# Performance work log

Measured on AMD Instinct MI355X. Metric: run time of the kernel, lower is better.

Reference implementation:

```python
import jax, jax.numpy as jnp
import numpy as np

SIGMA_MAX = 0.3
GAMMA = 1.0
COV_SHRINK = 0.1
COV_DELTA = 1e-3
BN_EPS = 1e-5
PATCH = 3


def setup_inputs() -> dict:
    key = jax.random.key(0)
    ks = jax.random.split(key, 5)
    B, K, C, H, W = 2, 8, 64, 128, 128
    X = jax.random.normal(ks[0], (B, K, C, H, W), dtype=jnp.float32)
    w1 = jax.random.normal(ks[1], (C // 2, C), dtype=jnp.float32) * 0.1
    w2 = jax.random.normal(ks[2], (1, C // 2), dtype=jnp.float32) * 0.1
    return {
        "X": X,
        "w1": w1,
        "bn_scale": jnp.ones((C // 2,), jnp.float32),
        "bn_bias": jnp.zeros((C // 2,), jnp.float32),
        "bn_mean": jnp.zeros((C // 2,), jnp.float32),
        "bn_var": jnp.ones((C // 2,), jnp.float32),
        "w2": w2,
        "a0_raw": jax.random.normal(ks[3], (K,), dtype=jnp.float32) * 0.1,
        "sigma_raw": jax.random.normal(ks[4], (K,), dtype=jnp.float32) * 0.1,
    }


def _forward(X, w1, bn_scale, bn_bias, bn_mean, bn_var, w2, a0_raw, sigma_raw):
    B, K, C, H, W = X.shape
    # --- SensorMapGenerator: 1x1 conv -> BN (inference) -> ReLU -> 1x1 conv ---
    Xf = X.reshape(B * K, C, H, W)
    h = jnp.einsum('oc,bchw->bohw', w1, Xf)                       # [BK, C/2, H, W]
    inv_std = bn_scale / jnp.sqrt(bn_var + BN_EPS)
    h = h * inv_std[None, :, None, None] + (bn_bias - bn_mean * inv_std)[None, :, None, None]
    h = jax.nn.relu(h)
    S = jnp.einsum('oc,bchw->bohw', w2, h).reshape(B, K, H, W)    # scalar sensor maps

    # --- CovarianceEstimator: reflect pad, 3x3 patches, center, R = PP^T/N ---
    pad = PATCH // 2
    Sp = jnp.pad(S, ((0, 0), (0, 0), (pad, pad), (pad, pad)), mode='reflect')
    patches = jnp.stack(
        [Sp[:, :, i:i + H, j:j + W] for i in range(PATCH) for j in range(PATCH)],
        axis=-1)                                                  # [B, K, H, W, N]
    N = PATCH * PATCH
    patches = patches.transpose(0, 2, 3, 1, 4)                    # [B, H, W, K, N]
    pc = patches - patches.mean(axis=-1, keepdims=True)
    R = jnp.matmul(pc, pc.swapaxes(-1, -2)) / N                   # [B, H, W, K, K]

    # --- Guidance vector and uncertainty (stage mode) ---
    a0 = jax.nn.softmax(a0_raw)                                   # [K], sums to 1
    sigma = SIGMA_MAX * jax.nn.sigmoid(sigma_raw)                 # [K]

    # --- Robust diagonal-loaded Capon solve per pixel ---
    # R_reg = (1-shrink)*R + shrink*(tr R / K)*I + delta*I + gamma*diag(sigma^2)
    I = jnp.eye(K, dtype=R.dtype)
    tr = jnp.trace(R, axis1=-2, axis2=-1)                         # [B, H, W]
    load = COV_DELTA * I + GAMMA * jnp.diag(sigma * sigma)
    R_load = (1.0 - COV_SHRINK) * R + (COV_SHRINK * tr / K)[..., None, None] * I + load
    rhs = jnp.broadcast_to(a0[:, None], R_load.shape[:-2] + (K, 1))
    w_un = jnp.linalg.solve(R_load, rhs)[..., 0]                  # [B, H, W, K]
    denom = jnp.einsum('bhwk,k->bhw', w_un, a0)
    w = w_un / denom[..., None]                                   # a0^T w = 1

    # --- Weighted fusion over streams ---
    Y = jnp.einsum('bhwk,bkchw->bchw', w, X)                      # [B, C, H, W]
    return Y


def reference(X, w1, bn_scale, bn_bias, bn_mean, bn_var, w2, a0_raw, sigma_raw):
    return _forward(X, w1, bn_scale, bn_bias, bn_mean, bn_var, w2, a0_raw, sigma_raw)
```

## Files before the change

### kernel.cpp

```cpp
#include <hip/hip_runtime.h>
#include <hip/hip_bf16.h>
#include <math.h>

#define B_    2
#define K_    8
#define C_    64
#define CH_   32
#define H_    128
#define W_    128
#define HW_   16384
#define BN_EPS 1e-5f
#define SIGMA_MAX 0.3f
#define COV_SHRINK 0.1f
#define COV_DELTA 1e-3f

#define REP32(M) \
    M(0)  M(1)  M(2)  M(3)  M(4)  M(5)  M(6)  M(7)  \
    M(8)  M(9)  M(10) M(11) M(12) M(13) M(14) M(15) \
    M(16) M(17) M(18) M(19) M(20) M(21) M(22) M(23) \
    M(24) M(25) M(26) M(27) M(28) M(29) M(30) M(31)

__global__ void prep_kernel(const float* __restrict__ w1,
                            const float* __restrict__ bn_scale,
                            const float* __restrict__ bn_bias,
                            const float* __restrict__ bn_mean,
                            const float* __restrict__ bn_var,
                            const float* __restrict__ w2,
                            float* __restrict__ par) {
    int t = threadIdx.x;
    for (int i = t; i < CH_ * C_; i += blockDim.x) {
        int c = i >> 5;
        int o = i & 31;
        float inv = bn_scale[o] * rsqrtf(bn_var[o] + BN_EPS);
        par[c * CH_ + o] = w1[o * C_ + c] * inv;
    }
    if (t < CH_) {
        float inv = bn_scale[t] * rsqrtf(bn_var[t] + BN_EPS);
        par[2048 + t] = bn_bias[t] - bn_mean[t] * inv;
        par[2080 + t] = w2[t];
    }
}

__global__ void __launch_bounds__(256)
stage1_kernel(const float* __restrict__ X,
              const float* __restrict__ wf,
              const float* __restrict__ beff,
              const float* __restrict__ w2c,
              float* __restrict__ S) {
    int idx = blockIdx.x * blockDim.x + threadIdx.x;
    int hw = idx & (HW_ - 1);
    int bk = idx >> 14;
    const float* xp = X + (size_t)bk * (C_ * HW_) + hw;

#define DECL_ACC(o) float a##o = beff[o];
    REP32(DECL_ACC)
#undef DECL_ACC

#pragma unroll 2
    for (int c = 0; c < C_; ++c) {
        float xv = xp[(size_t)c * HW_];
        const float* wr = wf + c * CH_;
#define FMA_ONE(o) a##o = fmaf(wr[o], xv, a##o);
        REP32(FMA_ONE)
#undef FMA_ONE
    }

    float s = 0.f;
#define REDUCE_ONE(o) s = fmaf(w2c[o], fmaxf(a##o, 0.f), s);
    REP32(REDUCE_ONE)
#undef REDUCE_ONE
    S[idx] = s;
}

__global__ void capon_kernel(const float* __restrict__ S,
                             const float* __restrict__ a0_raw,
                             const float* __restrict__ sigma_raw,
                             float* __restrict__ wOut) {
    int idx = blockIdx.x * blockDim.x + threadIdx.x;
    int b  = idx >> 14;
    int hw = idx & (HW_ - 1);
    int h  = hw >> 7;
    int w  = hw & (W_ - 1);

    float a0[K_], sig2[K_];
    {
        float m = -1e30f;
#pragma unroll
        for (int i = 0; i < K_; ++i) m = fmaxf(m, a0_raw[i]);
        float sum = 0.f;
#pragma unroll
        for (int i = 0; i < K_; ++i) { a0[i] = __expf(a0_raw[i] - m); sum += a0[i]; }
        float invs = 1.f / sum;
#pragma unroll
        for (int i = 0; i < K_; ++i) a0[i] *= invs;
#pragma unroll
        for (int i = 0; i < K_; ++i) {
            float sg = SIGMA_MAX / (1.f + __expf(-sigma_raw[i]));
            sig2[i] = sg * sg;
        }
    }

    int hm = (h == 0)      ? 1       : h - 1;
    int hp = (h == H_ - 1) ? H_ - 2  : h + 1;
    int wm = (w == 0)      ? 1       : w - 1;
    int wp = (w == W_ - 1) ? W_ - 2  : w + 1;
    int rows[3] = {hm * W_, h * W_, hp * W_};
    int cols[3] = {wm, w, wp};

    float pc[K_][9];
#pragma unroll
    for (int k = 0; k < K_; ++k) {
        const float* sp = S + (((size_t)b * K_ + k) << 14);
        float p[9];
        float m = 0.f;
#pragma unroll
        for (int i = 0; i < 3; ++i)
#pragma unroll
            for (int j = 0; j < 3; ++j) {
                float v = sp[rows[i] + cols[j]];
                p[i * 3 + j] = v;
                m += v;
            }
        m *= (1.f / 9.f);
#pragma unroll
        for (int n = 0; n < 9; ++n) pc[k][n] = p[n] - m;
    }

    float A[K_][K_];
    float tr = 0.f;
#pragma unroll
    for (int i = 0; i < K_; ++i) {
        float s = 0.f;
#pragma unroll
        for (int n = 0; n < 9; ++n) s = fmaf(pc[i][n], pc[i][n], s);
        s *= (1.f / 9.f);
        tr += s;
        A[i][i] = s;
    }
#pragma unroll
    for (int i = 0; i < K_; ++i)
#pragma unroll
        for (int j = 0; j < i; ++j) {
            float s = 0.f;
#pragma unroll
            for (int n = 0; n < 9; ++n) s = fmaf(pc[i][n], pc[j][n], s);
            A[i][j] = (1.f - COV_SHRINK) * s * (1.f / 9.f);
        }
    float dl = COV_SHRINK * tr * (1.f / (float)K_) + COV_DELTA;
#pragma unroll
    for (int i = 0; i < K_; ++i)
        A[i][i] = (1.f - COV_SHRINK) * A[i][i] + dl + sig2[i];

#pragma unroll
    for (int j = 0; j < K_; ++j) {
        float d = A[j][j];
#pragma unroll
        for (int t = 0; t < j; ++t) d = fmaf(-A[j][t], A[j][t], d);
        d = sqrtf(d);
        A[j][j] = d;
        float inv = 1.f / d;
#pragma unroll
        for (int i = j + 1; i < K_; ++i) {
            float s = A[i][j];
#pragma unroll
            for (int t = 0; t < j; ++t) s = fmaf(-A[i][t], A[j][t], s);
            A[i][j] = s * inv;
        }
    }
    float z[K_];
#pragma unroll
    for (int i = 0; i < K_; ++i) {
        float s = a0[i];
#pragma unroll
        for (int t = 0; t < i; ++t) s = fmaf(-A[i][t], z[t], s);
        z[i] = s / A[i][i];
    }
    float x[K_];
#pragma unroll
    for (int i = K_ - 1; i >= 0; --i) {
        float s = z[i];
#pragma unroll
        for (int t = i + 1; t < K_; ++t) s = fmaf(-A[t][i], x[t], s);
        x[i] = s / A[i][i];
    }
    float denom = 0.f;
#pragma unroll
    for (int k = 0; k < K_; ++k) denom = fmaf(x[k], a0[k], denom);
    float invd = 1.f / denom;

    float4 o0 = make_float4(x[0] * invd, x[1] * invd, x[2] * invd, x[3] * invd);
    float4 o1 = make_float4(x[4] * invd, x[5] * invd, x[6] * invd, x[7] * invd);
    float4* dst = (float4*)(wOut + (size_t)idx * K_);
    dst[0] = o0;
    dst[1] = o1;
}

__global__ void __launch_bounds__(256)
fuse_kernel(const float* __restrict__ X,
            const float* __restrict__ wW,
            float* __restrict__ out) {
    int idx = blockIdx.x * blockDim.x + threadIdx.x;
    int hw = idx & (HW_ - 1);
    int bc = idx >> 14;
    int b = bc >> 6;
    int c = bc & (C_ - 1);
    size_t pix = ((size_t)b << 14) + hw;

    const float4* wv4 = (const float4*)(wW + pix * K_);
    float4 wa = wv4[0];
    float4 wb = wv4[1];

    const float* xp = X + (((size_t)b * K_) * C_ + c) * HW_ + hw;
    const size_t kstride = (size_t)C_ * HW_;

    float acc;
    acc = wa.x * xp[0];
    acc = fmaf(wa.y, xp[kstride * 1], acc);
    acc = fmaf(wa.z, xp[kstride * 2], acc);
    acc = fmaf(wa.w, xp[kstride * 3], acc);
    acc = fmaf(wb.x, xp[kstride * 4], acc);
    acc = fmaf(wb.y, xp[kstride * 5], acc);
    acc = fmaf(wb.z, xp[kstride * 6], acc);
    acc = fmaf(wb.w, xp[kstride * 7], acc);
    __builtin_nontemporal_store(acc, &out[idx]);
}

extern "C" void kernel_launch(void* const* d_in, const int* in_sizes, int n_in,
                              void* d_out, int out_size, void* d_ws, size_t ws_size,
                              hipStream_t stream) {
    const float* X         = (const float*)d_in[0];
    const float* w1        = (const float*)d_in[1];
    const float* bn_scale  = (const float*)d_in[2];
    const float* bn_bias   = (const float*)d_in[3];
    const float* bn_mean   = (const float*)d_in[4];
    const float* bn_var    = (const float*)d_in[5];
    const float* w2        = (const float*)d_in[6];
    const float* a0_raw    = (const float*)d_in[7];
    const float* sigma_raw = (const float*)d_in[8];
    float* out = (float*)d_out;
    float* ws  = (float*)d_ws;

    float* par = ws;
    float* S   = ws + 4096;
    float* wW  = ws + 4096 + (B_ * K_ * HW_);

    prep_kernel<<<1, 256, 0, stream>>>(w1, bn_scale, bn_bias, bn_mean, bn_var,
                                       w2, par);

    int n1 = B_ * K_ * HW_;
    stage1_kernel<<<n1 / 256, 256, 0, stream>>>(X, par, par + 2048, par + 2080, S);

    int n2 = B_ * HW_;
    capon_kernel<<<n2 / 64, 64, 0, stream>>>(S, a0_raw, sigma_raw, wW);

    int n3 = B_ * C_ * HW_;
    fuse_kernel<<<n3 / 256, 256, 0, stream>>>(X, wW, out);
}
```

Baseline: 141.0 us.

## Fuse Capon solve with stream fusion and process two pixels per stage1 thread

The Capon kernel now does the weighted fusion over streams itself. Each thread loops over all 64 channels, using its per-pixel weights kept in registers. This removes the separate fuse kernel launch and the round trip of the weight buffer through global memory. Stage1 is also changed so each thread handles two adjacent pixels with float2 loads, reusing each loaded weight for two FMAs. The risk is that the memory-bound fusion pass, which reads all of X, now runs on only 32K threads in 64-thread blocks, which may leave too few loads in flight to cover latency.

```diff
diff --git a/kernel.cpp b/kernel.cpp
--- a/kernel.cpp
+++ b/kernel.cpp
@@ -47,35 +47,38 @@
               const float* __restrict__ beff,
               const float* __restrict__ w2c,
               float* __restrict__ S) {
-    int idx = blockIdx.x * blockDim.x + threadIdx.x;
-    int hw = idx & (HW_ - 1);
-    int bk = idx >> 14;
-    const float* xp = X + (size_t)bk * (C_ * HW_) + hw;
-
-#define DECL_ACC(o) float a##o = beff[o];
+    int t = blockIdx.x * blockDim.x + threadIdx.x;
+    int hw2 = t & (HW_ / 2 - 1);
+    int bk  = t >> 13;
+    const float2* xp = (const float2*)(X + (size_t)bk * (C_ * HW_)) + hw2;
+
+#define DECL_ACC(o) float u##o = beff[o]; float v##o = u##o;
     REP32(DECL_ACC)
 #undef DECL_ACC
 
-#pragma unroll 2
+#pragma unroll 4
     for (int c = 0; c < C_; ++c) {
-        float xv = xp[(size_t)c * HW_];
+        float2 xv = xp[(size_t)c * (HW_ / 2)];
         const float* wr = wf + c * CH_;
-#define FMA_ONE(o) a##o = fmaf(wr[o], xv, a##o);
+#define FMA_ONE(o) u##o = fmaf(wr[o], xv.x, u##o); v##o = fmaf(wr[o], xv.y, v##o);
         REP32(FMA_ONE)
 #undef FMA_ONE
     }
 
-    float s = 0.f;
-#define REDUCE_ONE(o) s = fmaf(w2c[o], fmaxf(a##o, 0.f), s);
+    float s0 = 0.f, s1 = 0.f;
+#define REDUCE_ONE(o) \
+    s0 = fmaf(w2c[o], fmaxf(u##o, 0.f), s0); \
+    s1 = fmaf(w2c[o], fmaxf(v##o, 0.f), s1);
     REP32(REDUCE_ONE)
 #undef REDUCE_ONE
-    S[idx] = s;
-}
-
-__global__ void capon_kernel(const float* __restrict__ S,
-                             const float* __restrict__ a0_raw,
-                             const float* __restrict__ sigma_raw,
-                             float* __restrict__ wOut) {
+    ((float2*)S)[t] = make_float2(s0, s1);
+}
+
+__global__ void capon_fuse_kernel(const float* __restrict__ S,
+                                  const float* __restrict__ a0_raw,
+                                  const float* __restrict__ sigma_raw,
+                                  const float* __restrict__ X,
+                                  float* __restrict__ out) {
     int idx = blockIdx.x * blockDim.x + threadIdx.x;
     int b  = idx >> 14;
     int hw = idx & (HW_ - 1);
@@ -188,41 +191,27 @@
     for (int k = 0; k < K_; ++k) denom = fmaf(x[k], a0[k], denom);
     float invd = 1.f / denom;
 
-    float4 o0 = make_float4(x[0] * invd, x[1] * invd, x[2] * invd, x[3] * invd);
-    float4 o1 = make_float4(x[4] * invd, x[5] * invd, x[6] * invd, x[7] * invd);
-    float4* dst = (float4*)(wOut + (size_t)idx * K_);
-    dst[0] = o0;
-    dst[1] = o1;
-}
-
-__global__ void __launch_bounds__(256)
-fuse_kernel(const float* __restrict__ X,
-            const float* __restrict__ wW,
-            float* __restrict__ out) {
-    int idx = blockIdx.x * blockDim.x + threadIdx.x;
-    int hw = idx & (HW_ - 1);
-    int bc = idx >> 14;
-    int b = bc >> 6;
-    int c = bc & (C_ - 1);
-    size_t pix = ((size_t)b << 14) + hw;
-
-    const float4* wv4 = (const float4*)(wW + pix * K_);
-    float4 wa = wv4[0];
-    float4 wb = wv4[1];
-
-    const float* xp = X + (((size_t)b * K_) * C_ + c) * HW_ + hw;
-    const size_t kstride = (size_t)C_ * HW_;
-
-    float acc;
-    acc = wa.x * xp[0];
-    acc = fmaf(wa.y, xp[kstride * 1], acc);
-    acc = fmaf(wa.z, xp[kstride * 2], acc);
-    acc = fmaf(wa.w, xp[kstride * 3], acc);
-    acc = fmaf(wb.x, xp[kstride * 4], acc);
-    acc = fmaf(wb.y, xp[kstride * 5], acc);
-    acc = fmaf(wb.z, xp[kstride * 6], acc);
-    acc = fmaf(wb.w, xp[kstride * 7], acc);
-    __builtin_nontemporal_store(acc, &out[idx]);
+    float wk[K_];
+#pragma unroll
+    for (int k = 0; k < K_; ++k) wk[k] = x[k] * invd;
+
+    const float* xb = X + ((size_t)b * K_) * (C_ * HW_) + hw;
+    float* ob = out + ((size_t)b * C_) * HW_ + hw;
+    const size_t KS = (size_t)C_ * HW_;
+
+#pragma unroll 4
+    for (int c = 0; c < C_; ++c) {
+        const float* xc = xb + (size_t)c * HW_;
+        float acc = wk[0] * xc[0];
+        acc = fmaf(wk[1], xc[KS * 1], acc);
+        acc = fmaf(wk[2], xc[KS * 2], acc);
+        acc = fmaf(wk[3], xc[KS * 3], acc);
+        acc = fmaf(wk[4], xc[KS * 4], acc);
+        acc = fmaf(wk[5], xc[KS * 5], acc);
+        acc = fmaf(wk[6], xc[KS * 6], acc);
+        acc = fmaf(wk[7], xc[KS * 7], acc);
+        __builtin_nontemporal_store(acc, ob + (size_t)c * HW_);
+    }
 }
 
 extern "C" void kernel_launch(void* const* d_in, const int* in_sizes, int n_in,
@@ -242,17 +231,13 @@
 
     float* par = ws;
     float* S   = ws + 4096;
-    float* wW  = ws + 4096 + (B_ * K_ * HW_);
 
     prep_kernel<<<1, 256, 0, stream>>>(w1, bn_scale, bn_bias, bn_mean, bn_var,
                                        w2, par);
 
-    int n1 = B_ * K_ * HW_;
+    int n1 = B_ * K_ * HW_ / 2;
     stage1_kernel<<<n1 / 256, 256, 0, stream>>>(X, par, par + 2048, par + 2080, S);
 
     int n2 = B_ * HW_;
-    capon_kernel<<<n2 / 64, 64, 0, stream>>>(S, a0_raw, sigma_raw, wW);
-
-    int n3 = B_ * C_ * HW_;
-    fuse_kernel<<<n3 / 256, 256, 0, stream>>>(X, wW, out);
-}
+    capon_fuse_kernel<<<n2 / 64, 64, 0, stream>>>(S, a0_raw, sigma_raw, X, out);
+}
```

After: 143.6 us. Within noise of the previous version (+1.9%).
